# Kernel optimization log

Hardware: AMD Instinct MI355X
Metric: run time of the kernel (lower is better)

## Reference

```python
import jax, jax.numpy as jnp
import numpy as np

TOP_P = 0.95        # sample() default topp
TEMPERATURE = 0.8   # token_temperature
NEG_INF = float('-inf')


def setup_inputs() -> dict:
    key = jax.random.key(0)
    k1, k2 = jax.random.split(key)
    B, V = 8192, 2048  # batch rows x speech-unit vocab
    logits = jax.random.normal(k1, (B, V), dtype=jnp.float32) * 4.0
    # uniform noise for Gumbel-max multinomial sampling (open interval)
    u = jax.random.uniform(k2, (B, V), dtype=jnp.float32, minval=1e-6, maxval=1.0 - 1e-6)
    return {"logits": logits, "u": u}


def _top_p_filter(logits, p):
    # descending sort (matches torch.sort(descending=True))
    order = jnp.argsort(-logits, axis=-1)                      # [B, V]
    sorted_logits = jnp.take_along_axis(logits, order, axis=-1)
    cum = jnp.cumsum(jax.nn.softmax(sorted_logits, axis=-1), axis=-1)
    remove = cum > p
    # shift right by one so the first token above the threshold is kept
    remove = jnp.concatenate(
        [jnp.zeros_like(remove[..., :1]), remove[..., :-1]], axis=-1)
    # scatter mask back to unsorted order via inverse permutation
    inv = jnp.argsort(order, axis=-1)
    remove_unsorted = jnp.take_along_axis(remove, inv, axis=-1)
    return jnp.where(remove_unsorted, NEG_INF, logits)


def reference(logits, u):
    scaled = logits / TEMPERATURE
    filtered = _top_p_filter(scaled, TOP_P)                    # [B, V]
    probs = jax.nn.softmax(filtered, axis=-1)                  # [B, V]
    # multinomial(probs, 1) == Gumbel-max over filtered logits
    gumbel = -jnp.log(-jnp.log(u))
    sampled = jnp.argmax(filtered + gumbel, axis=-1, keepdims=True)  # [B, 1]
    return sampled, probs
```

## Files before the change

kernel.cpp:

```cpp
#include <hip/hip_runtime.h>
#include <math.h>

#define VOCAB 2048
#define TPB   256
#define NBINS 64
#define BIN_SCALE 6.0f

typedef float vf4 __attribute__((ext_vector_type(4)));

__global__ __launch_bounds__(TPB, 8) void sampler_kernel(
    const float* __restrict__ logits,
    const float* __restrict__ uni,
    float* __restrict__ out_idx,
    float* __restrict__ out_probs)
{
    const int row  = blockIdx.x;
    const int t    = threadIdx.x;
    const int lane = t & 63;
    const int wid  = t >> 6;

    __shared__ float  s_bins[NBINS];
    __shared__ float  s_wf[4];
    __shared__ double s_wd[4];
    __shared__ float  s_wk[4];
    __shared__ unsigned long long s_key[4];
    __shared__ double s_S, s_cumBefore;
    __shared__ int    s_bstar, s_cnt, s_cnt2;
    __shared__ float  s_cv[VOCAB];
    __shared__ float  s_ce[VOCAB];

    const float* lrow = logits    + (size_t)row * VOCAB;
    const float* urow = uni       + (size_t)row * VOCAB;
    float*       prow = out_probs + (size_t)row * VOCAB;

    if (t < NBINS) s_bins[t] = 0.0f;
    if (t == 0)    { s_cnt = 0; s_cnt2 = 0; }

    const vf4 a0 = *(const vf4*)(lrow + 4 * t);
    const vf4 a1 = *(const vf4*)(lrow + VOCAB / 2 + 4 * t);
    float s[8] = {a0.x * 1.25f, a0.y * 1.25f, a0.z * 1.25f, a0.w * 1.25f,
                  a1.x * 1.25f, a1.y * 1.25f, a1.z * 1.25f, a1.w * 1.25f};

    float lm = s[0];
    #pragma unroll
    for (int j = 1; j < 8; j++) lm = fmaxf(lm, s[j]);
    #pragma unroll
    for (int off = 32; off; off >>= 1) lm = fmaxf(lm, __shfl_down(lm, off));
    if (lane == 0) s_wf[wid] = lm;
    __syncthreads();
    const float m = fmaxf(fmaxf(s_wf[0], s_wf[1]), fmaxf(s_wf[2], s_wf[3]));

    float e[8];
    int   bin[8];
    float psum = 0.0f;
    #pragma unroll
    for (int j = 0; j < 8; j++) {
        e[j] = __expf(s[j] - m);
        psum += e[j];
        bin[j] = (int)((m - s[j]) * BIN_SCALE);
        if (bin[j] < NBINS) atomicAdd(&s_bins[bin[j]], e[j]);
    }
    double dp = (double)psum;
    #pragma unroll
    for (int off = 32; off; off >>= 1) dp += __shfl_down(dp, off);
    if (lane == 0) s_wd[wid] = dp;
    __syncthreads();

    if (wid == 0) {
        double S  = s_wd[0] + s_wd[1] + s_wd[2] + s_wd[3];
        float  bf = s_bins[lane];
        double c  = (double)bf;
        #pragma unroll
        for (int d = 1; d < 64; d <<= 1) {
            double o = __shfl_up(c, d);
            if (lane >= d) c += o;
        }
        double pS = 0.95 * S;
        unsigned long long ball = __ballot(c > pS);
        int bstar = ball ? (__ffsll(ball) - 1) : (NBINS - 1);
        double excl = c - (double)bf;
        double cumB = __shfl(excl, bstar);
        if (lane == 0) { s_S = S; s_bstar = bstar; s_cumBefore = cumB; }
    }
    __syncthreads();
    const double pS        = 0.95 * s_S;
    const int    bstar     = s_bstar;
    const double cumBefore = s_cumBefore;

    #pragma unroll
    for (int j = 0; j < 8; j++) {
        if (bin[j] == bstar) {
            int pos = atomicAdd(&s_cnt, 1);
            s_cv[pos] = s[j];
            s_ce[pos] = e[j];
        }
    }
    __syncthreads();
    const int cnt = s_cnt;

    unsigned keptMask = 0;
    float    kpsum    = 0.0f;
    #pragma unroll
    for (int j = 0; j < 8; j++) {
        bool kept;
        if (bin[j] < bstar)      kept = true;
        else if (bin[j] > bstar) kept = false;
        else {
            float part = 0.0f;
            for (int i = 0; i < cnt; i++)
                if (s_cv[i] > s[j]) part += s_ce[i];
            kept = (cumBefore + (double)part) <= pS;
        }
        if (kept) { keptMask |= (1u << j); kpsum += e[j]; }
    }
    #pragma unroll
    for (int off = 32; off; off >>= 1) kpsum += __shfl_down(kpsum, off);
    if (lane == 0) s_wk[wid] = kpsum;
    __syncthreads();
    const float SK    = s_wk[0] + s_wk[1] + s_wk[2] + s_wk[3];
    const float invSK = 1.0f / SK;

    vf4 p0, p1;
    p0.x = (keptMask & 0x01) ? e[0] * invSK : 0.0f;
    p0.y = (keptMask & 0x02) ? e[1] * invSK : 0.0f;
    p0.z = (keptMask & 0x04) ? e[2] * invSK : 0.0f;
    p0.w = (keptMask & 0x08) ? e[3] * invSK : 0.0f;
    p1.x = (keptMask & 0x10) ? e[4] * invSK : 0.0f;
    p1.y = (keptMask & 0x20) ? e[5] * invSK : 0.0f;
    p1.z = (keptMask & 0x40) ? e[6] * invSK : 0.0f;
    p1.w = (keptMask & 0x80) ? e[7] * invSK : 0.0f;
    __builtin_nontemporal_store(p0, (vf4*)(prow + 4 * t));
    __builtin_nontemporal_store(p1, (vf4*)(prow + VOCAB / 2 + 4 * t));

    #pragma unroll
    for (int j = 0; j < 8; j++) {
        if ((keptMask >> j) & 1u) {
            int idx = (j < 4) ? (4 * t + j) : (VOCAB / 2 + 4 * t + (j - 4));
            int pos = atomicAdd(&s_cnt2, 1);
            s_cv[pos] = s[j];
            s_ce[pos] = __int_as_float(idx);
        }
    }
    __syncthreads();
    const int k = s_cnt2;

    unsigned long long key = 0ull;
    for (int i = t; i < k; i += TPB) {
        float sv  = s_cv[i];
        int   idx = __float_as_int(s_ce[i]);
        float uv  = urow[idx];
        float g   = -logf(-logf(uv));
        float z   = sv + g;
        unsigned zb = __float_as_uint(z);
        zb = (zb & 0x80000000u) ? ~zb : (zb | 0x80000000u);
        unsigned long long kk =
            ((unsigned long long)zb << 32) | (unsigned)(VOCAB - 1 - idx);
        key = (kk > key) ? kk : key;
    }
    #pragma unroll
    for (int off = 32; off; off >>= 1) {
        unsigned long long ok = __shfl_down(key, off);
        key = (ok > key) ? ok : key;
    }
    if (lane == 0) s_key[wid] = key;
    __syncthreads();
    if (t == 0) {
        unsigned long long k0 = s_key[0];
        #pragma unroll
        for (int w = 1; w < 4; w++) k0 = (s_key[w] > k0) ? s_key[w] : k0;
        out_idx[row] = (float)(VOCAB - 1 - (int)(k0 & 0xFFFFFFFFu));
    }
}

extern "C" void kernel_launch(void* const* d_in, const int* in_sizes, int n_in,
                              void* d_out, int out_size, void* d_ws, size_t ws_size,
                              hipStream_t stream) {
    const float* logits = (const float*)d_in[0];
    const float* u      = (const float*)d_in[1];
    const int B = in_sizes[0] / VOCAB;
    float* out_idx   = (float*)d_out;
    float* out_probs = (float*)d_out + B;
    sampler_kernel<<<B, TPB, 0, stream>>>(logits, u, out_idx, out_probs);
}
```

Before: 164.7 us.

## Process one row per wavefront to eliminate block-level synchronization

```diff
diff --git a/kernel.cpp b/kernel.cpp
--- a/kernel.cpp
+++ b/kernel.cpp
@@ -3,151 +3,149 @@
 
 #define VOCAB 2048
 #define TPB   256
+#define RPB   4
 #define NBINS 64
 #define BIN_SCALE 6.0f
+#define CAP   512
 
 typedef float vf4 __attribute__((ext_vector_type(4)));
 
-__global__ __launch_bounds__(TPB, 8) void sampler_kernel(
+__global__ __launch_bounds__(TPB, 4) void sampler_kernel(
     const float* __restrict__ logits,
     const float* __restrict__ uni,
     float* __restrict__ out_idx,
     float* __restrict__ out_probs)
 {
-    const int row  = blockIdx.x;
-    const int t    = threadIdx.x;
-    const int lane = t & 63;
-    const int wid  = t >> 6;
+    const int lane = threadIdx.x & 63;
+    const int wid  = threadIdx.x >> 6;
+    const int row  = (blockIdx.x << 2) | wid;
 
-    __shared__ float  s_bins[NBINS];
-    __shared__ float  s_wf[4];
-    __shared__ double s_wd[4];
-    __shared__ float  s_wk[4];
-    __shared__ unsigned long long s_key[4];
-    __shared__ double s_S, s_cumBefore;
-    __shared__ int    s_bstar, s_cnt, s_cnt2;
-    __shared__ float  s_cv[VOCAB];
-    __shared__ float  s_ce[VOCAB];
+    __shared__ float s_bins[RPB][NBINS];
+    __shared__ float s_cv[RPB][CAP];
+    __shared__ float s_ci[RPB][CAP];
+    __shared__ int   s_bcnt[RPB];
+    __shared__ int   s_kcnt[RPB];
 
     const float* lrow = logits    + (size_t)row * VOCAB;
     const float* urow = uni       + (size_t)row * VOCAB;
     float*       prow = out_probs + (size_t)row * VOCAB;
 
-    if (t < NBINS) s_bins[t] = 0.0f;
-    if (t == 0)    { s_cnt = 0; s_cnt2 = 0; }
+    s_bins[wid][lane] = 0.0f;
+    if (lane == 0) { s_bcnt[wid] = 0; s_kcnt[wid] = 0; }
 
-    const vf4 a0 = *(const vf4*)(lrow + 4 * t);
-    const vf4 a1 = *(const vf4*)(lrow + VOCAB / 2 + 4 * t);
-    float s[8] = {a0.x * 1.25f, a0.y * 1.25f, a0.z * 1.25f, a0.w * 1.25f,
-                  a1.x * 1.25f, a1.y * 1.25f, a1.z * 1.25f, a1.w * 1.25f};
-
-    float lm = s[0];
-    #pragma unroll
-    for (int j = 1; j < 8; j++) lm = fmaxf(lm, s[j]);
-    #pragma unroll
-    for (int off = 32; off; off >>= 1) lm = fmaxf(lm, __shfl_down(lm, off));
-    if (lane == 0) s_wf[wid] = lm;
-    __syncthreads();
-    const float m = fmaxf(fmaxf(s_wf[0], s_wf[1]), fmaxf(s_wf[2], s_wf[3]));
-
-    float e[8];
-    int   bin[8];
-    float psum = 0.0f;
+    float s[32];
     #pragma unroll
     for (int j = 0; j < 8; j++) {
+        vf4 a = __builtin_nontemporal_load((const vf4*)(lrow + j * 256 + 4 * lane));
+        s[4*j+0] = a.x * 1.25f;
+        s[4*j+1] = a.y * 1.25f;
+        s[4*j+2] = a.z * 1.25f;
+        s[4*j+3] = a.w * 1.25f;
+    }
+
+    float m0 = s[0], m1 = s[1], m2 = s[2], m3 = s[3];
+    #pragma unroll
+    for (int j = 4; j < 32; j += 4) {
+        m0 = fmaxf(m0, s[j+0]); m1 = fmaxf(m1, s[j+1]);
+        m2 = fmaxf(m2, s[j+2]); m3 = fmaxf(m3, s[j+3]);
+    }
+    float m = fmaxf(fmaxf(m0, m1), fmaxf(m2, m3));
+    #pragma unroll
+    for (int off = 32; off; off >>= 1)
+        m = fmaxf(m, __shfl_xor(m, off));
+
+    float e[32];
+    double p0 = 0.0, p1 = 0.0;
+    #pragma unroll
+    for (int j = 0; j < 32; j++) {
         e[j] = __expf(s[j] - m);
-        psum += e[j];
-        bin[j] = (int)((m - s[j]) * BIN_SCALE);
-        if (bin[j] < NBINS) atomicAdd(&s_bins[bin[j]], e[j]);
+        if (j & 1) p1 += (double)e[j]; else p0 += (double)e[j];
+        int b = (int)((m - s[j]) * BIN_SCALE);
+        if (b < NBINS) atomicAdd(&s_bins[wid][b], e[j]);
     }
-    double dp = (double)psum;
+    double dp = p0 + p1;
     #pragma unroll
-    for (int off = 32; off; off >>= 1) dp += __shfl_down(dp, off);
-    if (lane == 0) s_wd[wid] = dp;
-    __syncthreads();
+    for (int off = 32; off; off >>= 1)
+        dp += __shfl_xor(dp, off);
+    const double S  = dp;
+    const double pS = 0.95 * S;
 
-    if (wid == 0) {
-        double S  = s_wd[0] + s_wd[1] + s_wd[2] + s_wd[3];
-        float  bf = s_bins[lane];
-        double c  = (double)bf;
-        #pragma unroll
-        for (int d = 1; d < 64; d <<= 1) {
-            double o = __shfl_up(c, d);
-            if (lane >= d) c += o;
+    const float bf = s_bins[wid][lane];
+    double c = (double)bf;
+    #pragma unroll
+    for (int d = 1; d < 64; d <<= 1) {
+        double o = __shfl_up(c, d);
+        if (lane >= d) c += o;
+    }
+    const unsigned long long ball = __ballot(c > pS);
+    const int bstar = ball ? (__ffsll(ball) - 1) : (NBINS - 1);
+    double excl = c - (double)bf;
+    const double cumBefore = __shfl(excl, bstar);
+
+    #pragma unroll
+    for (int j = 0; j < 32; j++) {
+        int b = (int)((m - s[j]) * BIN_SCALE);
+        if (b == bstar) {
+            int pos = atomicAdd(&s_bcnt[wid], 1);
+            if (pos < CAP) { s_cv[wid][pos] = s[j]; s_ci[wid][pos] = e[j]; }
         }
-        double pS = 0.95 * S;
-        unsigned long long ball = __ballot(c > pS);
-        int bstar = ball ? (__ffsll(ball) - 1) : (NBINS - 1);
-        double excl = c - (double)bf;
-        double cumB = __shfl(excl, bstar);
-        if (lane == 0) { s_S = S; s_bstar = bstar; s_cumBefore = cumB; }
     }
-    __syncthreads();
-    const double pS        = 0.95 * s_S;
-    const int    bstar     = s_bstar;
-    const double cumBefore = s_cumBefore;
+    const int bcnt = min(s_bcnt[wid], CAP);
+
+    unsigned keptMask = 0;
+    float k0 = 0.0f, k1 = 0.0f;
+    #pragma unroll
+    for (int j = 0; j < 32; j++) {
+        int b = (int)((m - s[j]) * BIN_SCALE);
+        bool kept;
+        if (b < bstar)      kept = true;
+        else if (b > bstar) kept = false;
+        else {
+            float part = 0.0f;
+            for (int i = 0; i < bcnt; i++)
+                if (s_cv[wid][i] > s[j]) part += s_ci[wid][i];
+            kept = (cumBefore + (double)part) <= pS;
+        }
+        if (kept) {
+            keptMask |= (1u << j);
+            if (j & 1) k1 += e[j]; else k0 += e[j];
+        }
+    }
+    float kpsum = k0 + k1;
+    #pragma unroll
+    for (int off = 32; off; off >>= 1)
+        kpsum += __shfl_xor(kpsum, off);
+    const float invSK = 1.0f / kpsum;
 
     #pragma unroll
     for (int j = 0; j < 8; j++) {
-        if (bin[j] == bstar) {
-            int pos = atomicAdd(&s_cnt, 1);
-            s_cv[pos] = s[j];
-            s_ce[pos] = e[j];
+        vf4 p;
+        p.x = ((keptMask >> (4*j+0)) & 1u) ? e[4*j+0] * invSK : 0.0f;
+        p.y = ((keptMask >> (4*j+1)) & 1u) ? e[4*j+1] * invSK : 0.0f;
+        p.z = ((keptMask >> (4*j+2)) & 1u) ? e[4*j+2] * invSK : 0.0f;
+        p.w = ((keptMask >> (4*j+3)) & 1u) ? e[4*j+3] * invSK : 0.0f;
+        __builtin_nontemporal_store(p, (vf4*)(prow + j * 256 + 4 * lane));
+    }
+
+    unsigned ovf = 0;
+    #pragma unroll
+    for (int j = 0; j < 32; j++) {
+        if ((keptMask >> j) & 1u) {
+            int pos = atomicAdd(&s_kcnt[wid], 1);
+            if (pos < CAP) {
+                s_cv[wid][pos] = s[j];
+                s_ci[wid][pos] = __int_as_float((j >> 2) * 256 + 4 * lane + (j & 3));
+            } else {
+                ovf |= (1u << j);
+            }
         }
     }
-    __syncthreads();
-    const int cnt = s_cnt;
-
-    unsigned keptMask = 0;
-    float    kpsum    = 0.0f;
-    #pragma unroll
-    for (int j = 0; j < 8; j++) {
-        bool kept;
-        if (bin[j] < bstar)      kept = true;
-        else if (bin[j] > bstar) kept = false;
-        else {
-            float part = 0.0f;
-            for (int i = 0; i < cnt; i++)
-                if (s_cv[i] > s[j]) part += s_ce[i];
-            kept = (cumBefore + (double)part) <= pS;
-        }
-        if (kept) { keptMask |= (1u << j); kpsum += e[j]; }
-    }
-    #pragma unroll
-    for (int off = 32; off; off >>= 1) kpsum += __shfl_down(kpsum, off);
-    if (lane == 0) s_wk[wid] = kpsum;
-    __syncthreads();
-    const float SK    = s_wk[0] + s_wk[1] + s_wk[2] + s_wk[3];
-    const float invSK = 1.0f / SK;
-
-    vf4 p0, p1;
-    p0.x = (keptMask & 0x01) ? e[0] * invSK : 0.0f;
-    p0.y = (keptMask & 0x02) ? e[1] * invSK : 0.0f;
-    p0.z = (keptMask & 0x04) ? e[2] * invSK : 0.0f;
-    p0.w = (keptMask & 0x08) ? e[3] * invSK : 0.0f;
-    p1.x = (keptMask & 0x10) ? e[4] * invSK : 0.0f;
-    p1.y = (keptMask & 0x20) ? e[5] * invSK : 0.0f;
-    p1.z = (keptMask & 0x40) ? e[6] * invSK : 0.0f;
-    p1.w = (keptMask & 0x80) ? e[7] * invSK : 0.0f;
-    __builtin_nontemporal_store(p0, (vf4*)(prow + 4 * t));
-    __builtin_nontemporal_store(p1, (vf4*)(prow + VOCAB / 2 + 4 * t));
-
-    #pragma unroll
-    for (int j = 0; j < 8; j++) {
-        if ((keptMask >> j) & 1u) {
-            int idx = (j < 4) ? (4 * t + j) : (VOCAB / 2 + 4 * t + (j - 4));
-            int pos = atomicAdd(&s_cnt2, 1);
-            s_cv[pos] = s[j];
-            s_ce[pos] = __int_as_float(idx);
-        }
-    }
-    __syncthreads();
-    const int k = s_cnt2;
+    const int kc = min(s_kcnt[wid], CAP);
 
     unsigned long long key = 0ull;
-    for (int i = t; i < k; i += TPB) {
-        float sv  = s_cv[i];
-        int   idx = __float_as_int(s_ce[i]);
+    for (int i = lane; i < kc; i += 64) {
+        float sv  = s_cv[wid][i];
+        int   idx = __float_as_int(s_ci[wid][i]);
         float uv  = urow[idx];
         float g   = -logf(-logf(uv));
         float z   = sv + g;
@@ -157,19 +155,29 @@
             ((unsigned long long)zb << 32) | (unsigned)(VOCAB - 1 - idx);
         key = (kk > key) ? kk : key;
     }
+    if (__builtin_expect(ovf != 0, 0)) {
+        #pragma unroll
+        for (int j = 0; j < 32; j++) {
+            if ((ovf >> j) & 1u) {
+                int   idx = (j >> 2) * 256 + 4 * lane + (j & 3);
+                float uv  = urow[idx];
+                float g   = -logf(-logf(uv));
+                float z   = s[j] + g;
+                unsigned zb = __float_as_uint(z);
+                zb = (zb & 0x80000000u) ? ~zb : (zb | 0x80000000u);
+                unsigned long long kk =
+                    ((unsigned long long)zb << 32) | (unsigned)(VOCAB - 1 - idx);
+                key = (kk > key) ? kk : key;
+            }
+        }
+    }
     #pragma unroll
     for (int off = 32; off; off >>= 1) {
-        unsigned long long ok = __shfl_down(key, off);
+        unsigned long long ok = __shfl_xor(key, off);
         key = (ok > key) ? ok : key;
     }
-    if (lane == 0) s_key[wid] = key;
-    __syncthreads();
-    if (t == 0) {
-        unsigned long long k0 = s_key[0];
-        #pragma unroll
-        for (int w = 1; w < 4; w++) k0 = (s_key[w] > k0) ? s_key[w] : k0;
-        out_idx[row] = (float)(VOCAB - 1 - (int)(k0 & 0xFFFFFFFFu));
-    }
+    if (lane == 0)
+        out_idx[row] = (float)(VOCAB - 1 - (int)(key & 0xFFFFFFFFu));
 }
 
 extern "C" void kernel_launch(void* const* d_in, const int* in_sizes, int n_in,
@@ -180,5 +188,5 @@
     const int B = in_sizes[0] / VOCAB;
     float* out_idx   = (float*)d_out;
     float* out_probs = (float*)d_out + B;
-    sampler_kernel<<<B, TPB, 0, stream>>>(logits, u, out_idx, out_probs);
+    sampler_kernel<<<B / RPB, TPB, 0, stream>>>(logits, u, out_idx, out_probs);
 }
```

After: 169.7 us. 1.03x slower.
